# Optimization experiments

Hardware: AMD Instinct MI355X
Metric: run time of the kernel (lower is better)

Reference implementation:

```python
import jax, jax.numpy as jnp
import numpy as np


def setup_inputs() -> dict:
    key = jax.random.key(0)
    ks = jax.random.split(key, 8)
    B, T, N, F, H, E, P, O = 1, 24, 50000, 16, 64, 1600000, 5, 1
    sF = 1.0 / np.sqrt(F)
    sH = 1.0 / np.sqrt(H)
    return {
        "x_seq": jax.random.normal(ks[0], (B, T, N, F), jnp.float32),
        "edge_weight": jax.random.uniform(ks[1], (E,), jnp.float32),
        "gcn_w": jax.random.normal(ks[2], (F, H), jnp.float32) * sF,
        "gcn_b": jnp.zeros((H,), jnp.float32),
        "w_ih": jax.random.normal(ks[3], (3 * H, H), jnp.float32) * sH,
        "w_hh": jax.random.normal(ks[4], (3 * H, H), jnp.float32) * sH,
        "b_ih": jnp.zeros((3 * H,), jnp.float32),
        "b_hh": jnp.zeros((3 * H,), jnp.float32),
        "lin_w": jax.random.normal(ks[5], (P * O, H), jnp.float32) * sH,
        "lin_b": jnp.zeros((P * O,), jnp.float32),
        "edge_index": jax.random.randint(ks[6], (2, E), 0, N),
        "pred_horizons": P,
        "out_channels": O,
    }


def reference(x_seq, edge_weight, gcn_w, gcn_b, w_ih, w_hh, b_ih, b_hh,
              lin_w, lin_b, edge_index, pred_horizons, out_channels):
    B, T, N, F = x_seq.shape
    H = gcn_w.shape[1]
    src, dst = edge_index[0], edge_index[1]

    # GCNConv symmetric normalization with self-loops (weight 1).
    # NOTE: the original forward never passes edge_weight to GCNConv, so all
    # edge weights are 1 — edge_weight is accepted but unused, faithfully.
    deg = jax.ops.segment_sum(jnp.ones_like(src, x_seq.dtype), dst,
                              num_segments=N) + 1.0
    dinv = jax.lax.rsqrt(deg)
    norm = dinv[src] * dinv[dst]          # (E,)
    self_norm = dinv * dinv               # (N,) self-loop coefficient

    # GCNConv projects first, then aggregates.
    h = jnp.einsum('btnf,fh->btnh', x_seq, gcn_w)  # (B,T,N,H)

    def agg_one(h_t):  # (N, H) -> (N, H) sparse A_hat @ h_t
        msg = norm[:, None] * h_t[src]    # (E, H) gather
        return jax.ops.segment_sum(msg, dst, num_segments=N) \
            + self_norm[:, None] * h_t

    def agg_step(c, h_bt):  # h_bt: (B, N, H) — mirrors the per-timestep loop
        return c, jax.vmap(agg_one)(h_bt)

    _, g = jax.lax.scan(agg_step, 0, jnp.transpose(h, (1, 0, 2, 3)))  # (T,B,N,H)
    g = g + gcn_b

    # GRU over time per node: sequences of shape (B*N, T, H) -> scan over T.
    xs = g.reshape(T, B * N, H)

    def gru_step(hprev, x_t):
        gi = x_t @ w_ih.T + b_ih
        gh = hprev @ w_hh.T + b_hh
        i_r, i_z, i_n = jnp.split(gi, 3, axis=-1)
        h_r, h_z, h_n = jnp.split(gh, 3, axis=-1)
        r = jax.nn.sigmoid(i_r + h_r)
        z = jax.nn.sigmoid(i_z + h_z)
        n = jnp.tanh(i_n + r * h_n)
        return (1.0 - z) * n + z * hprev, None

    h_last, _ = jax.lax.scan(gru_step,
                             jnp.zeros((B * N, H), x_seq.dtype), xs)

    out = h_last @ lin_w.T + lin_b        # (B*N, P*O)
    out = out.reshape(B, N, pred_horizons, out_channels)
    return jnp.transpose(out, (0, 2, 1, 3))  # (B, P, N, O)
```

## Files before the change

kernel.cpp:

```cpp
#include <hip/hip_runtime.h>
#include <hip/hip_bf16.h>
#include <hip/hip_fp16.h>

#define TT 24
#define FF 16
#define HH 64
#define GG 192
#define ELLW 96
#define AROW 396

typedef __attribute__((ext_vector_type(4))) float f32x4;
typedef __attribute__((ext_vector_type(8))) _Float16 f16x8;

__device__ __forceinline__ float fast_rcp(float x){ return __builtin_amdgcn_rcpf(x); }
__device__ __forceinline__ float sigmoid_f(float x){
  return fast_rcp(1.0f + __expf(-x));
}
__device__ __forceinline__ float tanh_f(float x){
  float e = __expf(-2.0f * fabsf(x));
  float th = (1.0f - e) * fast_rcp(1.0f + e);
  return copysignf(th, x);
}
__device__ __forceinline__ uint pack_h2(float a, float b){
  ushort ha = __half_as_ushort(__float2half(a));
  ushort hb = __half_as_ushort(__float2half(b));
  return (uint)ha | ((uint)hb << 16);
}
__device__ __forceinline__ void acch8(__half2* a, uint4 u, __half2 wh){
  a[0] = __hfma2(*(__half2*)&u.x, wh, a[0]);
  a[1] = __hfma2(*(__half2*)&u.y, wh, a[1]);
  a[2] = __hfma2(*(__half2*)&u.z, wh, a[2]);
  a[3] = __hfma2(*(__half2*)&u.w, wh, a[3]);
}
__device__ __forceinline__ void acch4(__half2* a, uint2 u, __half2 wh){
  a[0] = __hfma2(*(__half2*)&u.x, wh, a[0]);
  a[1] = __hfma2(*(__half2*)&u.y, wh, a[1]);
}

__global__ __launch_bounds__(256)
void k_pre2(const float* __restrict__ x, ushort* __restrict__ xTh,
            const int* __restrict__ ei, int E, int* __restrict__ cnt, ushort* __restrict__ ell,
            const float* __restrict__ gcn_w, const float* __restrict__ gcn_b,
            const float* __restrict__ w_ih, const float* __restrict__ b_ih,
            const float* __restrict__ w_hh,
            ushort* __restrict__ m1F, float* __restrict__ c1, ushort* __restrict__ whhF,
            int N, int GX, int GD){
  __shared__ ushort tile[16][392];
  const int bid = blockIdx.x;
  const int tid = threadIdx.x;
  if(bid < GX){
    const int nbase = bid * 16;
    const int nd = tid >> 4, f = tid & 15;
    const int n = nbase + nd;
    for(int t=0; t<TT; t++){
      float v = (n < N) ? x[((size_t)t*N + n)*FF + f] : 0.f;
      tile[nd][t*16 + f] = __half_as_ushort(__float2half(v));
    }
    __syncthreads();
    uint* xo = (uint*)xTh;
    for(int i = tid; i < 16*192; i += 256){
      int d = i / 192, pos = i - d*192;
      int nn = nbase + d;
      if(nn < N) xo[(size_t)nn*192 + pos] = *(uint*)&tile[d][pos*2];
    }
  } else if(bid < GX + GD){
    int i = (bid - GX)*256 + tid;
    if(i < E){
      int s = ei[i], d = ei[E+i];
      int slot = atomicAdd(&cnt[d], 1);
      if(slot < ELLW) ell[(size_t)d*ELLW + slot] = (ushort)s;
    }
  } else {
    int t2 = (bid - GX - GD)*256 + tid;
    if(t2 < GG*FF){
      int j = t2 >> 4, f = t2 & 15;
      float s = 0.f;
      for(int k=0;k<HH;k++) s += gcn_w[f*HH+k]*w_ih[j*HH+k];
      m1F[t2] = __half_as_ushort(__float2half(s));
    } else if (t2 < GG*FF + GG){
      int j = t2 - GG*FF;
      float s = b_ih[j];
      for(int k=0;k<HH;k++) s += gcn_b[k]*w_ih[j*HH+k];
      c1[j] = s;
    }
    if(t2 < GG*HH){
      whhF[t2] = __half_as_ushort(__float2half(w_hh[t2]));
    }
  }
}

__global__ void k_dinvh(const int* __restrict__ cnt, ushort* __restrict__ dinvh, int N){
  int i = blockIdx.x*blockDim.x + threadIdx.x;
  if(i<N) dinvh[i] = __half_as_ushort(__float2half(rsqrtf((float)cnt[i] + 1.0f)));
}

__global__ __launch_bounds__(256, 4)
void k_fused(const ushort* __restrict__ xTh, const int* __restrict__ cnt,
             const ushort* __restrict__ ell, const ushort* __restrict__ dinvh,
             const ushort* __restrict__ whhF, const ushort* __restrict__ m1F,
             const float* __restrict__ c1, const float* __restrict__ bhh,
             const float* __restrict__ lin_w, const float* __restrict__ lin_b,
             float* __restrict__ out, int N, int P){
  __shared__ __align__(16) ushort agg_lds[16][AROW];
  __shared__ __align__(16) uint hb[2][512];
  __shared__ __align__(16) uint ell_w[4][48];
  const int tid = threadIdx.x;
  const int l = tid & 63, w = tid >> 6;
  const int half = l >> 5, lh = l & 31;
  const int nbase = blockIdx.x * 16;

  for(int i=tid; i<512; i+=256) hb[0][i]=0u;

  const ushort* myell = (const ushort*)ell_w[w];
  for(int q=0; q<4; q++){
    const int nl = w*4 + q;
    const int n = min(nbase + nl, N-1);
    __half2 hA[4], hB2[2];
    hA[0]=__half2{0,0}; hA[1]=__half2{0,0}; hA[2]=__half2{0,0}; hA[3]=__half2{0,0};
    hB2[0]=__half2{0,0}; hB2[1]=__half2{0,0};
    const __half dnh = __ushort_as_half(dinvh[n]);
    const int hi = min(cnt[n], ELLW);

    if(l < 48) ell_w[w][l] = *(const uint*)(ell + (uint)n*ELLW + l*2);

    for(int j = 0; j < hi; j += 8){
      int j0 = j     + half;
      int j1 = j + 2 + half;
      int j2 = j + 4 + half;
      int j3 = j + 6 + half;
      bool k0 = j0 < hi, k1 = j1 < hi, k2 = j2 < hi, k3 = j3 < hi;
      int s0 = n, s1 = n, s2 = n, s3 = n;
      if(k0) s0 = myell[j0];
      if(k1) s1 = myell[j1];
      if(k2) s2 = myell[j2];
      if(k3) s3 = myell[j3];
      __half z0 = __ushort_as_half((ushort)0);
      __half w0 = k0 ? __hmul(__ushort_as_half(dinvh[s0]), dnh) : z0;
      __half w1 = k1 ? __hmul(__ushort_as_half(dinvh[s1]), dnh) : z0;
      __half w2 = k2 ? __hmul(__ushort_as_half(dinvh[s2]), dnh) : z0;
      __half w3 = k3 ? __hmul(__ushort_as_half(dinvh[s3]), dnh) : z0;
      __half2 wh0 = __half2half2(w0);
      __half2 wh1 = __half2half2(w1);
      __half2 wh2 = __half2half2(w2);
      __half2 wh3 = __half2half2(w3);
      const ushort* r0 = xTh + (uint)s0*384u;
      const ushort* r1 = xTh + (uint)s1*384u;
      const ushort* r2 = xTh + (uint)s2*384u;
      const ushort* r3 = xTh + (uint)s3*384u;
      uint4 A0 = *(const uint4*)(r0 + lh*8);
      uint4 A1 = *(const uint4*)(r1 + lh*8);
      uint4 A2 = *(const uint4*)(r2 + lh*8);
      uint4 A3 = *(const uint4*)(r3 + lh*8);
      uint2 B0 = *(const uint2*)(r0 + 256 + lh*4);
      uint2 B1 = *(const uint2*)(r1 + 256 + lh*4);
      uint2 B2 = *(const uint2*)(r2 + 256 + lh*4);
      uint2 B3 = *(const uint2*)(r3 + 256 + lh*4);
      acch8(hA, A0, wh0); acch4(hB2, B0, wh0);
      acch8(hA, A1, wh1); acch4(hB2, B1, wh1);
      acch8(hA, A2, wh2); acch4(hB2, B2, wh2);
      acch8(hA, A3, wh3); acch4(hB2, B3, wh3);
    }
    #pragma unroll
    for(int k=0;k<4;k++){
      uint v = __shfl_xor(*(uint*)&hA[k], 32, 64);
      hA[k] = __hadd2(hA[k], *(__half2*)&v);
    }
    #pragma unroll
    for(int k=0;k<2;k++){
      uint v = __shfl_xor(*(uint*)&hB2[k], 32, 64);
      hB2[k] = __hadd2(hB2[k], *(__half2*)&v);
    }

    if(half == 0){
      __half2 snh = __half2half2(__hmul(dnh, dnh));
      const ushort* rS = xTh + (uint)n*384u;
      uint4 AS = *(const uint4*)(rS + lh*8);
      uint2 BS = *(const uint2*)(rS + 256 + lh*4);
      acch8(hA, AS, snh); acch4(hB2, BS, snh);
      ushort* row = &agg_lds[nl][0];
      uint4 h0;
      h0.x = *(uint*)&hA[0];
      h0.y = *(uint*)&hA[1];
      h0.z = *(uint*)&hA[2];
      h0.w = *(uint*)&hA[3];
      *(uint4*)(row + lh*8) = h0;
      uint2 hBo;
      hBo.x = *(uint*)&hB2[0];
      hBo.y = *(uint*)&hB2[1];
      *(uint2*)(row + 256 + lh*4) = hBo;
    }
  }
  __syncthreads();

  const int nd = l & 15, g = l >> 4;
  const int chB = 16*w;
  const f16x8 zf = (f16x8){0,0,0,0,0,0,0,0};
  f16x8 ar0,ar1,az0,az1,an0,an1, mr,mz,mn;
  {
    const int rr =        chB + nd;
    const int rz =  HH  + chB + nd;
    const int rn = 2*HH + chB + nd;
    ar0 = *(const f16x8*)(whhF + rr*HH      + g*8);
    ar1 = *(const f16x8*)(whhF + rr*HH + 32 + g*8);
    az0 = *(const f16x8*)(whhF + rz*HH      + g*8);
    az1 = *(const f16x8*)(whhF + rz*HH + 32 + g*8);
    an0 = *(const f16x8*)(whhF + rn*HH      + g*8);
    an1 = *(const f16x8*)(whhF + rn*HH + 32 + g*8);
    mr = zf; mz = zf; mn = zf;
    if(g < 2){
      mr = *(const f16x8*)(m1F + rr*FF + g*8);
      mz = *(const f16x8*)(m1F + rz*FF + g*8);
      mn = *(const f16x8*)(m1F + rn*FF + g*8);
    } else if(g == 2){
      mr[0] = (_Float16)(c1[rr] + bhh[rr]);
      mz[0] = (_Float16)(c1[rz] + bhh[rz]);
      mn[0] = (_Float16)(c1[rn]);
    }
  }
  float4 bb = *(const float4*)(bhh + 2*HH + chB + g*4);

  float hreg[4] = {0.f,0.f,0.f,0.f};
  f16x8 cB = zf;
  if(g==2) cB[0] = (_Float16)1.0f;

  const int swz = (nd & 7) << 2;

  for(int t=0; t<TT; t++){
    const uint* cb = hb[t & 1];
    uint* nb = hb[(t & 1) ^ 1];

    f16x8 hB0 = *(const f16x8*)(cb + nd*32 + ((g*4)      ^ swz));
    f16x8 hB1 = *(const f16x8*)(cb + nd*32 + ((16 + g*4) ^ swz));
    f16x8 cAg = cB;
    if(g < 2) cAg = *(const f16x8*)&agg_lds[nd][t*16 + g*8];

    f32x4 R  = {0.f,0.f,0.f,0.f};
    f32x4 Z  = {0.f,0.f,0.f,0.f};
    f32x4 Nh = {0.f,0.f,0.f,0.f};
    f32x4 Ni = {0.f,0.f,0.f,0.f};
    R  = __builtin_amdgcn_mfma_f32_16x16x32_f16(ar0, hB0, R , 0,0,0);
    R  = __builtin_amdgcn_mfma_f32_16x16x32_f16(ar1, hB1, R , 0,0,0);
    R  = __builtin_amdgcn_mfma_f32_16x16x32_f16(mr,  cAg, R , 0,0,0);
    Z  = __builtin_amdgcn_mfma_f32_16x16x32_f16(az0, hB0, Z , 0,0,0);
    Z  = __builtin_amdgcn_mfma_f32_16x16x32_f16(az1, hB1, Z , 0,0,0);
    Z  = __builtin_amdgcn_mfma_f32_16x16x32_f16(mz,  cAg, Z , 0,0,0);
    Nh = __builtin_amdgcn_mfma_f32_16x16x32_f16(an0, hB0, Nh, 0,0,0);
    Nh = __builtin_amdgcn_mfma_f32_16x16x32_f16(an1, hB1, Nh, 0,0,0);
    Ni = __builtin_amdgcn_mfma_f32_16x16x32_f16(mn,  cAg, Ni, 0,0,0);

    const float bbv[4] = {bb.x, bb.y, bb.z, bb.w};
    #pragma unroll
    for(int i=0;i<4;i++){
      float r_ = sigmoid_f(R[i]);
      float z_ = sigmoid_f(Z[i]);
      float nn = tanh_f(Ni[i] + r_*(Nh[i] + bbv[i]));
      hreg[i] = nn + z_*(hreg[i] - nn);
    }
    if(t+1 < TT){
      uint2 pk;
      pk.x = pack_h2(hreg[0], hreg[1]);
      pk.y = pack_h2(hreg[2], hreg[3]);
      *(uint2*)(nb + nd*32 + ((8*w + 2*g) ^ swz)) = pk;
      __syncthreads();
    }
  }

  __syncthreads();
  float* hs = (float*)hb;
  #pragma unroll
  for(int i=0;i<4;i++) hs[nd*64 + chB + g*4 + i] = hreg[i];
  __syncthreads();
  if(tid < 16*P){
    int ndl = tid & 15, p = tid >> 4;
    int node2 = nbase + ndl;
    if(node2 < N){
      float acc = lin_b[p];
      const float* hrow = hs + ndl*64;
      #pragma unroll
      for(int q=0;q<16;q++){
        float4 v = *(const float4*)(hrow + q*4);
        float4 lw = *(const float4*)(lin_w + p*HH + q*4);
        acc += v.x*lw.x + v.y*lw.y + v.z*lw.z + v.w*lw.w;
      }
      out[(size_t)p*N + node2] = acc;
    }
  }
}

extern "C" void kernel_launch(void* const* d_in, const int* in_sizes, int n_in,
                              void* d_out, int out_size, void* d_ws, size_t ws_size,
                              hipStream_t stream){
  const float* x     = (const float*)d_in[0];
  const float* gcn_w = (const float*)d_in[2];
  const float* gcn_b = (const float*)d_in[3];
  const float* w_ih  = (const float*)d_in[4];
  const float* w_hh  = (const float*)d_in[5];
  const float* b_ih  = (const float*)d_in[6];
  const float* b_hh  = (const float*)d_in[7];
  const float* lin_w = (const float*)d_in[8];
  const float* lin_b = (const float*)d_in[9];
  const int*   ei    = (const int*)d_in[10];
  const int E = in_sizes[10]/2;
  const int N = in_sizes[0]/(TT*FF);
  const int P = in_sizes[9];

  char* wsp = (char*)d_ws;
  auto alloc = [&](size_t bytes)->void*{ void* p = wsp; wsp += (bytes + 255) & ~(size_t)255; return p; };
  int*    cnt      = (int*)   alloc((size_t)N*4);
  ushort* dinvh    = (ushort*)alloc((size_t)N*2);
  ushort* ell      = (ushort*)alloc((size_t)N*ELLW*2);
  ushort* xTh      = (ushort*)alloc((size_t)N*384*2);
  ushort* m1F      = (ushort*)alloc((size_t)GG*FF*2);
  float*  c1       = (float*) alloc((size_t)GG*4);
  ushort* whhF     = (ushort*)alloc((size_t)GG*HH*2);

  hipMemsetAsync(cnt, 0, (size_t)N*4, stream);

  const int GX = (N + 15)/16;
  const int GD = (E + 255)/256;
  const int GP = (GG*HH + 255)/256;
  k_pre2 <<<GX + GD + GP, 256, 0, stream>>>(x, xTh, ei, E, cnt, ell,
                                            gcn_w, gcn_b, w_ih, b_ih, w_hh,
                                            m1F, c1, whhF, N, GX, GD);
  k_dinvh<<<(N+255)/256, 256, 0, stream>>>(cnt, dinvh, N);
  k_fused<<<(N+15)/16, 256, 0, stream>>>(xTh, cnt, ell, dinvh, whhF, m1F, c1, b_hh,
                                         lin_w, lin_b, (float*)d_out, N, P);
}
```

Baseline: 340.8 us.

## Pre-scale node features by dinv so edge aggregation becomes plain adds

Factors the symmetric GCN normalization by pre-multiplying each source node's fp16 feature row by its dinv in a separate pass. The inner edge loop then only sums gathered rows, with no per-edge dinv gathers or weight FMAs, and the destination dinv is applied once after the reduction. Masked edges point at a zero-filled padding row N instead of the node itself. The cost is an extra read-modify-write pass over the whole feature tensor and a slightly different fp16 rounding order.

```diff
diff --git a/kernel.cpp b/kernel.cpp
--- a/kernel.cpp
+++ b/kernel.cpp
@@ -26,15 +26,15 @@
   ushort hb = __half_as_ushort(__float2half(b));
   return (uint)ha | ((uint)hb << 16);
 }
-__device__ __forceinline__ void acch8(__half2* a, uint4 u, __half2 wh){
-  a[0] = __hfma2(*(__half2*)&u.x, wh, a[0]);
-  a[1] = __hfma2(*(__half2*)&u.y, wh, a[1]);
-  a[2] = __hfma2(*(__half2*)&u.z, wh, a[2]);
-  a[3] = __hfma2(*(__half2*)&u.w, wh, a[3]);
-}
-__device__ __forceinline__ void acch4(__half2* a, uint2 u, __half2 wh){
-  a[0] = __hfma2(*(__half2*)&u.x, wh, a[0]);
-  a[1] = __hfma2(*(__half2*)&u.y, wh, a[1]);
+__device__ __forceinline__ void adda8(__half2* a, uint4 u){
+  a[0] = __hadd2(a[0], *(__half2*)&u.x);
+  a[1] = __hadd2(a[1], *(__half2*)&u.y);
+  a[2] = __hadd2(a[2], *(__half2*)&u.z);
+  a[3] = __hadd2(a[3], *(__half2*)&u.w);
+}
+__device__ __forceinline__ void adda4(__half2* a, uint2 u){
+  a[0] = __hadd2(a[0], *(__half2*)&u.x);
+  a[1] = __hadd2(a[1], *(__half2*)&u.y);
 }
 
 __global__ __launch_bounds__(256)
@@ -89,9 +89,21 @@
   }
 }
 
-__global__ void k_dinvh(const int* __restrict__ cnt, ushort* __restrict__ dinvh, int N){
+__global__ void k_scale(const int* __restrict__ cnt, ushort* __restrict__ xTh,
+                        ushort* __restrict__ dinvh, int N){
   int i = blockIdx.x*blockDim.x + threadIdx.x;
-  if(i<N) dinvh[i] = __half_as_ushort(__float2half(rsqrtf((float)cnt[i] + 1.0f)));
+  int total = (N+1)*192;
+  if(i >= total) return;
+  int n = i / 192, d = i - n*192;
+  uint* p = (uint*)xTh;
+  if(n >= N){ p[i] = 0u; return; }
+  float dv = rsqrtf((float)cnt[n] + 1.0f);
+  __half2 dh2 = __half2half2(__float2half(dv));
+  uint v = p[i];
+  __half2 hv = *(__half2*)&v;
+  hv = __hmul2(hv, dh2);
+  p[i] = *(uint*)&hv;
+  if(d == 0) dinvh[n] = __half_as_ushort(__float2half(dv));
 }
 
 __global__ __launch_bounds__(256, 4)
@@ -129,20 +141,11 @@
       int j2 = j + 4 + half;
       int j3 = j + 6 + half;
       bool k0 = j0 < hi, k1 = j1 < hi, k2 = j2 < hi, k3 = j3 < hi;
-      int s0 = n, s1 = n, s2 = n, s3 = n;
+      int s0 = N, s1 = N, s2 = N, s3 = N;
       if(k0) s0 = myell[j0];
       if(k1) s1 = myell[j1];
       if(k2) s2 = myell[j2];
       if(k3) s3 = myell[j3];
-      __half z0 = __ushort_as_half((ushort)0);
-      __half w0 = k0 ? __hmul(__ushort_as_half(dinvh[s0]), dnh) : z0;
-      __half w1 = k1 ? __hmul(__ushort_as_half(dinvh[s1]), dnh) : z0;
-      __half w2 = k2 ? __hmul(__ushort_as_half(dinvh[s2]), dnh) : z0;
-      __half w3 = k3 ? __hmul(__ushort_as_half(dinvh[s3]), dnh) : z0;
-      __half2 wh0 = __half2half2(w0);
-      __half2 wh1 = __half2half2(w1);
-      __half2 wh2 = __half2half2(w2);
-      __half2 wh3 = __half2half2(w3);
       const ushort* r0 = xTh + (uint)s0*384u;
       const ushort* r1 = xTh + (uint)s1*384u;
       const ushort* r2 = xTh + (uint)s2*384u;
@@ -155,10 +158,10 @@
       uint2 B1 = *(const uint2*)(r1 + 256 + lh*4);
       uint2 B2 = *(const uint2*)(r2 + 256 + lh*4);
       uint2 B3 = *(const uint2*)(r3 + 256 + lh*4);
-      acch8(hA, A0, wh0); acch4(hB2, B0, wh0);
-      acch8(hA, A1, wh1); acch4(hB2, B1, wh1);
-      acch8(hA, A2, wh2); acch4(hB2, B2, wh2);
-      acch8(hA, A3, wh3); acch4(hB2, B3, wh3);
+      adda8(hA, A0); adda4(hB2, B0);
+      adda8(hA, A1); adda4(hB2, B1);
+      adda8(hA, A2); adda4(hB2, B2);
+      adda8(hA, A3); adda4(hB2, B3);
     }
     #pragma unroll
     for(int k=0;k<4;k++){
@@ -172,11 +175,15 @@
     }
 
     if(half == 0){
-      __half2 snh = __half2half2(__hmul(dnh, dnh));
       const ushort* rS = xTh + (uint)n*384u;
       uint4 AS = *(const uint4*)(rS + lh*8);
       uint2 BS = *(const uint2*)(rS + 256 + lh*4);
-      acch8(hA, AS, snh); acch4(hB2, BS, snh);
+      adda8(hA, AS); adda4(hB2, BS);
+      __half2 dnh2 = __half2half2(dnh);
+      #pragma unroll
+      for(int k=0;k<4;k++) hA[k] = __hmul2(hA[k], dnh2);
+      #pragma unroll
+      for(int k=0;k<2;k++) hB2[k] = __hmul2(hB2[k], dnh2);
       ushort* row = &agg_lds[nl][0];
       uint4 h0;
       h0.x = *(uint*)&hA[0];
@@ -309,7 +316,7 @@
   int*    cnt      = (int*)   alloc((size_t)N*4);
   ushort* dinvh    = (ushort*)alloc((size_t)N*2);
   ushort* ell      = (ushort*)alloc((size_t)N*ELLW*2);
-  ushort* xTh      = (ushort*)alloc((size_t)N*384*2);
+  ushort* xTh      = (ushort*)alloc((size_t)(N+1)*384*2);
   ushort* m1F      = (ushort*)alloc((size_t)GG*FF*2);
   float*  c1       = (float*) alloc((size_t)GG*4);
   ushort* whhF     = (ushort*)alloc((size_t)GG*HH*2);
@@ -322,7 +329,7 @@
   k_pre2 <<<GX + GD + GP, 256, 0, stream>>>(x, xTh, ei, E, cnt, ell,
                                             gcn_w, gcn_b, w_ih, b_ih, w_hh,
                                             m1F, c1, whhF, N, GX, GD);
-  k_dinvh<<<(N+255)/256, 256, 0, stream>>>(cnt, dinvh, N);
+  k_scale<<<((N+1)*192 + 255)/256, 256, 0, stream>>>(cnt, xTh, dinvh, N);
   k_fused<<<(N+15)/16, 256, 0, stream>>>(xTh, cnt, ell, dinvh, whhF, m1F, c1, b_hh,
                                          lin_w, lin_b, (float*)d_out, N, P);
 }
```

Measured after the change: 325.9 us (median of 2 runs). -4.4%, faster.
